# Performance work log

Hardware: AMD Instinct MI355X
Metric: run time of the kernel (lower is better)

## Reference

```python
import jax, jax.numpy as jnp
from jax import lax
import numpy as np

B, T, D, UNITS, NCLASSES = 256, 256, 512, 1024, 512


def setup_inputs() -> dict:
    key = jax.random.key(0)
    ks = jax.random.split(key, 6)
    x = jax.random.normal(ks[0], (B, T, D), dtype=jnp.float32)
    W = jax.random.normal(ks[1], (D + NCLASSES, 4 * UNITS), dtype=jnp.float32) * 0.02
    U = jax.random.normal(ks[2], (UNITS, 4 * UNITS), dtype=jnp.float32) * 0.02
    b = jnp.zeros((4 * UNITS,), dtype=jnp.float32)
    Wout = jax.random.normal(ks[3], (UNITS, NCLASSES), dtype=jnp.float32) * 0.02
    bout = jnp.zeros((NCLASSES,), dtype=jnp.float32)
    return {"x": x, "W": W, "U": U, "b": b, "Wout": Wout, "bout": bout}


def _hard_sigmoid(z):
    # Keras LSTM default recurrent activation
    return jnp.clip(0.2 * z + 0.5, 0.0, 1.0)


def reference(x, W, U, b, Wout, bout):
    units = U.shape[0]
    nclasses = Wout.shape[1]
    batch = x.shape[0]

    def step(carry, x_t):
        word_vec, h, c = carry
        ins = jnp.concatenate([x_t, word_vec], axis=1)          # [B, D+nclasses]
        z = ins @ W + h @ U + b                                  # [B, 4*units]
        zi, zf, zc, zo = jnp.split(z, 4, axis=1)
        c_new = _hard_sigmoid(zf) * c + _hard_sigmoid(zi) * jnp.tanh(zc)
        h_new = _hard_sigmoid(zo) * jnp.tanh(c_new)
        probs = jax.nn.softmax(h_new @ Wout + bout, axis=1)      # [B, nclasses]
        idx = jnp.argmax(probs, axis=1)                          # [B]
        new_word = jax.nn.one_hot(idx, nclasses, dtype=x_t.dtype)
        return (new_word, h_new, c_new), idx

    x_tmajor = jnp.swapaxes(x, 0, 1)                             # [T, B, D]
    # start_word = zeros_like(x_shuffled[0]) -> [B, D] (D == nclasses)
    init = (jnp.zeros((batch, x.shape[2]), x.dtype),
            jnp.zeros((batch, units), x.dtype),
            jnp.zeros((batch, units), x.dtype))
    _, idxs = lax.scan(step, init, x_tmajor)                     # [T, B]
    return jnp.swapaxes(idxs, 0, 1)                              # [B, T]
```

## Files before the change

### kernel.cpp

```cpp
#include <hip/hip_runtime.h>
#include <math.h>
#include <stdint.h>

#define Bn 256
#define Tn 256
#define Dn 512
#define UNITSn 1024
#define NCn 512
#define G4n 4096
#define KTn 1536
#define NT 48

typedef unsigned long long u64;
typedef __attribute__((ext_vector_type(4))) double d4;

__device__ __forceinline__ double hsigd(double z) {
    return fmin(fmax(0.2 * z + 0.5, 0.0), 1.0);
}

__device__ __forceinline__ u64 packlc(double v, int col) {
    double s = (v + 2048.0) * 1099511627776.0;
    u64 q = (u64)s;
    return (q << 10) | (u64)(1023 - col);
}

__global__ void convert_weights(const float* __restrict__ W, const float* __restrict__ U,
                                double* __restrict__ Wd)
{
    size_t stride = (size_t)gridDim.x * blockDim.x;
    for (size_t i = (size_t)blockIdx.x * blockDim.x + threadIdx.x;
         i < (size_t)KTn * G4n; i += stride) {
        int k = (int)(i >> 12);
        int j = (int)(i & 4095);
        float v = (k < Dn) ? W[i] : U[(size_t)(k - Dn) * G4n + j];
        Wd[i] = (double)v;
    }
}

#define AS_STR 34
#define BS_STR 34
#define AS_TILE (64 * AS_STR)
#define BS_TILE (32 * BS_STR)

__global__ __launch_bounds__(256, 2) void lstm_step_mfma(
    const float* __restrict__ x, const double* __restrict__ Wd,
    const float* __restrict__ W, const float* __restrict__ bias,
    const double* __restrict__ hin, double* __restrict__ hout,
    double* __restrict__ cst,
    const u64* __restrict__ slots_prev, u64* __restrict__ slots_cur,
    int* __restrict__ out, int t)
{
    __shared__ __align__(16) double smem[2 * AS_TILE + 2 * BS_TILE];

    const int tid = threadIdx.x;
    const int bid = blockIdx.x;
    const int ct_ = bid & 127;
    const int yt = bid >> 7;
    const int u0 = ct_ * 8;
    const int rowbase = yt * 64;

    if (ct_ == 0 && tid < 64) slots_cur[rowbase + tid] = 0ull;

    const int sr = tid >> 2;
    const int sk0 = (tid & 3) * 8;
    const int lb_k = tid >> 3;
    const int lb_c4 = (tid & 7) * 4;
    const int lb_gate = lb_c4 >> 3;
    const int lb_uoff = lb_c4 & 7;

    const float* xrow = x + (size_t)(rowbase + sr) * (Tn * Dn) + (size_t)t * Dn;
    const double* hrow = hin + (size_t)(rowbase + sr) * UNITSn;
    const double* wb = Wd + (size_t)lb_gate * UNITSn + u0 + lb_uoff;

    double apf[8];
    double2 bpf[2];

    auto prefetch = [&](int it) {
        int k0 = it * 32 + sk0;
        if (k0 < Dn) {
            float4 v0 = *(const float4*)(xrow + k0);
            float4 v1 = *(const float4*)(xrow + k0 + 4);
            apf[0] = (double)v0.x; apf[1] = (double)v0.y;
            apf[2] = (double)v0.z; apf[3] = (double)v0.w;
            apf[4] = (double)v1.x; apf[5] = (double)v1.y;
            apf[6] = (double)v1.z; apf[7] = (double)v1.w;
        } else {
            const double* hp = hrow + (k0 - Dn);
            double2 a = *(const double2*)(hp + 0);
            double2 b = *(const double2*)(hp + 2);
            double2 c2 = *(const double2*)(hp + 4);
            double2 d = *(const double2*)(hp + 6);
            apf[0] = a.x; apf[1] = a.y; apf[2] = b.x; apf[3] = b.y;
            apf[4] = c2.x; apf[5] = c2.y; apf[6] = d.x; apf[7] = d.y;
        }
        const double* bp = wb + (size_t)(it * 32 + lb_k) * G4n;
        bpf[0] = *(const double2*)(bp);
        bpf[1] = *(const double2*)(bp + 2);
    };
    auto store_tiles = [&](int p) {
        double* As = smem + p * AS_TILE;
        double* Bs = smem + 2 * AS_TILE + p * BS_TILE;
        #pragma unroll
        for (int j = 0; j < 8; j += 2) {
            double2 w2; w2.x = apf[j]; w2.y = apf[j + 1];
            *(double2*)&As[sr * AS_STR + sk0 + j] = w2;
        }
        *(double2*)&Bs[lb_k * BS_STR + lb_c4] = bpf[0];
        *(double2*)&Bs[lb_k * BS_STR + lb_c4 + 2] = bpf[1];
    };

    const int lane = tid & 63;
    const int wvi = tid >> 6;
    const int rs = wvi * 16;
    const int ml = lane & 15;
    const int kl = lane >> 4;

    d4 zero4 = {0.0, 0.0, 0.0, 0.0};
    double onek0 = (kl == 0) ? 1.0 : 0.0;
    double mk0   = (kl == 0) ? (double)ml : 0.0;
    d4 prow = __builtin_amdgcn_mfma_f64_16x16x4f64(mk0, onek0, zero4, 0, 0, 0);
    d4 pcol = __builtin_amdgcn_mfma_f64_16x16x4f64(onek0, mk0, zero4, 0, 0, 0);
    int zoff[4];
    #pragma unroll
    for (int r = 0; r < 4; r++)
        zoff[r] = (rs + (int)prow[r]) * 33 + (int)pcol[r];

    d4 acc[2];
    acc[0] = zero4; acc[1] = zero4;

    prefetch(0);
    store_tiles(0);
    __syncthreads();

    int p = 0;
    for (int it = 0; it < NT; it++) {
        if (it + 1 < NT) prefetch(it + 1);
        {
            const double* As = smem + p * AS_TILE;
            const double* Bs = smem + 2 * AS_TILE + p * BS_TILE;
            #pragma unroll
            for (int kq = 0; kq < 8; kq++) {
                double a = As[(rs + ml) * AS_STR + kq * 4 + kl];
                double b0 = Bs[(kq * 4 + kl) * BS_STR + ml];
                double b1 = Bs[(kq * 4 + kl) * BS_STR + 16 + ml];
                acc[0] = __builtin_amdgcn_mfma_f64_16x16x4f64(a, b0, acc[0], 0, 0, 0);
                acc[1] = __builtin_amdgcn_mfma_f64_16x16x4f64(a, b1, acc[1], 0, 0, 0);
            }
        }
        if (it + 1 < NT) store_tiles(p ^ 1);
        __syncthreads();
        p ^= 1;
    }

    double* zex = smem;
    #pragma unroll
    for (int r = 0; r < 4; r++) {
        zex[zoff[r]] = acc[0][r];
        zex[zoff[r] + 16] = acc[1][r];
    }
    __syncthreads();

    const int eu = tid & 7;
    const int rr = tid >> 3;
    const int ug = u0 + eu;
    const double bi0 = (double)bias[ug];
    const double bf0 = (double)bias[UNITSn + ug];
    const double bc0 = (double)bias[2 * UNITSn + ug];
    const double bo0 = (double)bias[3 * UNITSn + ug];

    #pragma unroll
    for (int s = 0; s < 2; s++) {
        int r = rr + 32 * s;
        int row = rowbase + r;
        double zi = zex[r * 33 + eu]      + bi0;
        double zf = zex[r * 33 + 8 + eu]  + bf0;
        double zc = zex[r * 33 + 16 + eu] + bc0;
        double zo = zex[r * 33 + 24 + eu] + bo0;
        if (t > 0) {
            u64 sp = slots_prev[row];
            int idx = 1023 - (int)(sp & 1023ull);
            const float* wrow = W + (size_t)(Dn + idx) * G4n + ug;
            zi += (double)wrow[0];
            zf += (double)wrow[UNITSn];
            zc += (double)wrow[2 * UNITSn];
            zo += (double)wrow[3 * UNITSn];
            if (ct_ == 0 && eu == 0) out[(size_t)row * Tn + (t - 1)] = idx;
        }
        size_t off = (size_t)row * UNITSn + ug;
        double cold = cst[off];
        double ig = hsigd(zi), fg = hsigd(zf), og = hsigd(zo);
        double cn = fg * cold + ig * tanh(zc);
        double hn = og * tanh(cn);
        cst[off] = cn;
        hout[off] = hn;
    }
}

__global__ __launch_bounds__(256, 2) void lstm_step(
    const float* __restrict__ x, const float* __restrict__ W,
    const float* __restrict__ U, const float* __restrict__ bias,
    const double* __restrict__ hin, double* __restrict__ hout,
    double* __restrict__ cst,
    const u64* __restrict__ slots_prev, u64* __restrict__ slots_cur,
    int* __restrict__ out, int t)
{
    __shared__ __align__(16) double smem[6144];

    const int tid = threadIdx.x;
    const int bid = blockIdx.x;
    const int ut = bid & 127;
    const int yt = bid >> 7;
    const int u0 = ut * 8;
    const int rowbase = yt * 64;

    if (ut == 0 && tid < 64) slots_cur[rowbase + tid] = 0ull;

    const int la_row = tid >> 2;
    const int la_k0 = (tid & 3) * 8;
    const int lb_k  = tid >> 3;
    const int lb_c4 = (tid & 7) * 4;
    const int lb_gate = lb_c4 >> 3;
    const int lb_uoff = lb_c4 & 7;

    const float* xrow = x + (size_t)(rowbase + la_row) * (Tn * Dn) + (size_t)t * Dn;
    const double* hrow = hin + (size_t)(rowbase + la_row) * UNITSn;

    double a_pf[8];
    double b_pf[4];

    auto prefetch = [&](int it) {
        int kg = it * 32;
        int k0 = kg + la_k0;
        if (k0 < Dn) {
            float4 v0 = *(const float4*)(xrow + k0);
            float4 v1 = *(const float4*)(xrow + k0 + 4);
            a_pf[0] = (double)v0.x; a_pf[1] = (double)v0.y;
            a_pf[2] = (double)v0.z; a_pf[3] = (double)v0.w;
            a_pf[4] = (double)v1.x; a_pf[5] = (double)v1.y;
            a_pf[6] = (double)v1.z; a_pf[7] = (double)v1.w;
        } else {
            const double* hp = hrow + (k0 - Dn);
            double2 h0v = *(const double2*)(hp + 0);
            double2 h1v = *(const double2*)(hp + 2);
            double2 h2v = *(const double2*)(hp + 4);
            double2 h3v = *(const double2*)(hp + 6);
            a_pf[0] = h0v.x; a_pf[1] = h0v.y; a_pf[2] = h1v.x; a_pf[3] = h1v.y;
            a_pf[4] = h2v.x; a_pf[5] = h2v.y; a_pf[6] = h3v.x; a_pf[7] = h3v.y;
        }
        int kB = kg + lb_k;
        const float* rowp = (kB < Dn) ? (W + (size_t)kB * G4n)
                                      : (U + (size_t)(kB - Dn) * G4n);
        float4 wv = *(const float4*)(rowp + lb_gate * UNITSn + u0 + lb_uoff);
        b_pf[0] = (double)wv.x; b_pf[1] = (double)wv.y;
        b_pf[2] = (double)wv.z; b_pf[3] = (double)wv.w;
    };
    auto store_tiles = [&](int p) {
        double* As = smem + p * 2048;
        double* Bs = smem + 4096 + p * 1024;
        #pragma unroll
        for (int j = 0; j < 8; j++) As[(la_k0 + j) * 64 + la_row] = a_pf[j];
        double2 w0; w0.x = b_pf[0]; w0.y = b_pf[1];
        double2 w1; w1.x = b_pf[2]; w1.y = b_pf[3];
        *(double2*)&Bs[lb_k * 32 + lb_c4] = w0;
        *(double2*)&Bs[lb_k * 32 + lb_c4 + 2] = w1;
    };

    const int lane = tid & 63;
    const int wv_ = tid >> 6;
    const int ri = lane >> 3;
    const int cj = lane & 7;
    const int rb = wv_ * 16 + ri * 2;

    double acc[2][4];
    #pragma unroll
    for (int i = 0; i < 2; i++)
        #pragma unroll
        for (int j = 0; j < 4; j++) acc[i][j] = 0.0;

    prefetch(0);
    store_tiles(0);
    __syncthreads();

    int p = 0;
    for (int it = 0; it < NT; it++) {
        if (it + 1 < NT) prefetch(it + 1);
        {
            const double* As = smem + p * 2048;
            const double* Bs = smem + 4096 + p * 1024;
            #pragma unroll
            for (int k = 0; k < 32; k++) {
                double2 a2 = *(const double2*)&As[k * 64 + rb];
                double2 b0 = *(const double2*)&Bs[k * 32 + cj * 4];
                double2 b1 = *(const double2*)&Bs[k * 32 + cj * 4 + 2];
                acc[0][0] = fma(a2.x, b0.x, acc[0][0]);
                acc[0][1] = fma(a2.x, b0.y, acc[0][1]);
                acc[0][2] = fma(a2.x, b1.x, acc[0][2]);
                acc[0][3] = fma(a2.x, b1.y, acc[0][3]);
                acc[1][0] = fma(a2.y, b0.x, acc[1][0]);
                acc[1][1] = fma(a2.y, b0.y, acc[1][1]);
                acc[1][2] = fma(a2.y, b1.x, acc[1][2]);
                acc[1][3] = fma(a2.y, b1.y, acc[1][3]);
            }
        }
        if (it + 1 < NT) store_tiles(p ^ 1);
        __syncthreads();
        p ^= 1;
    }

    double* zex = smem;
    #pragma unroll
    for (int i = 0; i < 2; i++) {
        double2 z0; z0.x = acc[i][0]; z0.y = acc[i][1];
        double2 z1; z1.x = acc[i][2]; z1.y = acc[i][3];
        *(double2*)&zex[(rb + i) * 32 + cj * 4] = z0;
        *(double2*)&zex[(rb + i) * 32 + cj * 4 + 2] = z1;
    }
    __syncthreads();

    const int eu = tid & 7;
    const int rr = tid >> 3;
    const int ug = u0 + eu;
    const double bi0 = (double)bias[ug];
    const double bf0 = (double)bias[UNITSn + ug];
    const double bc0 = (double)bias[2 * UNITSn + ug];
    const double bo0 = (double)bias[3 * UNITSn + ug];

    #pragma unroll
    for (int s = 0; s < 2; s++) {
        int r = rr + 32 * s;
        int row = rowbase + r;
        double zi = zex[r * 32 + eu]      + bi0;
        double zf = zex[r * 32 + 8 + eu]  + bf0;
        double zc = zex[r * 32 + 16 + eu] + bc0;
        double zo = zex[r * 32 + 24 + eu] + bo0;
        if (t > 0) {
            u64 sp = slots_prev[row];
            int idx = 1023 - (int)(sp & 1023ull);
            const float* wrow = W + (size_t)(Dn + idx) * G4n + ug;
            zi += (double)wrow[0];
            zf += (double)wrow[UNITSn];
            zc += (double)wrow[2 * UNITSn];
            zo += (double)wrow[3 * UNITSn];
            if (ut == 0 && eu == 0) out[(size_t)row * Tn + (t - 1)] = idx;
        }
        size_t off = (size_t)row * UNITSn + ug;
        double cold = cst[off];
        double ig = hsigd(zi), fg = hsigd(zf), og = hsigd(zo);
        double cn = fg * cold + ig * tanh(zc);
        double hn = og * tanh(cn);
        cst[off] = cn;
        hout[off] = hn;
    }
}

#define C_RT 8
#define C_CT 64
#define C_KC 32

__global__ __launch_bounds__(256) void logits_argmax(
    const double* __restrict__ h, const float* __restrict__ Wout,
    const float* __restrict__ bout, u64* __restrict__ slots)
{
    __shared__ double Hs[C_KC][9];
    __shared__ float  Ws[C_KC][C_CT];

    const int tid = threadIdx.x;
    const int ty = tid >> 5;
    const int tx = tid & 31;
    const int rbase = blockIdx.y * C_RT;
    const int cbase = blockIdx.x * C_CT;

    double acc0 = 0.0, acc1 = 0.0;

    const int lh_row = tid >> 5;
    const int lh_kk = tid & 31;
    const int lw_kk = tid >> 4;
    const int lw_j0 = (tid & 15) * 4;

    for (int kb = 0; kb < UNITSn; kb += C_KC) {
        Hs[lh_kk][lh_row] = h[(size_t)(rbase + lh_row) * UNITSn + kb + lh_kk];
        #pragma unroll
        for (int it = 0; it < 2; it++) {
            int kk = lw_kk + it * 16;
            float4 v = *(const float4*)(Wout + (size_t)(kb + kk) * NCn + cbase + lw_j0);
            *(float4*)&Ws[kk][lw_j0] = v;
        }
        __syncthreads();
        #pragma unroll
        for (int kk = 0; kk < C_KC; kk++) {
            double a = Hs[kk][ty];
            float2 wv = *(const float2*)&Ws[kk][tx * 2];
            acc0 = fma(a, (double)wv.x, acc0);
            acc1 = fma(a, (double)wv.y, acc1);
        }
        __syncthreads();
    }

    int col0 = cbase + tx * 2;
    double lg0 = acc0 + (double)bout[col0];
    double lg1 = acc1 + (double)bout[col0 + 1];

    u64 p0 = packlc(lg0, col0);
    u64 p1 = packlc(lg1, col0 + 1);
    u64 best = (p0 > p1) ? p0 : p1;
    #pragma unroll
    for (int off = 16; off >= 1; off >>= 1) {
        u64 o = __shfl_down(best, off, 32);
        if (o > best) best = o;
    }
    if (tx == 0) atomicMax(&slots[rbase + ty], best);
}

__global__ void final_decode(const u64* __restrict__ slots, int* __restrict__ out) {
    int b = threadIdx.x;
    u64 s = slots[b];
    out[(size_t)b * Tn + (Tn - 1)] = 1023 - (int)(s & 1023ull);
}

extern "C" void kernel_launch(void* const* d_in, const int* in_sizes, int n_in,
                              void* d_out, int out_size, void* d_ws, size_t ws_size,
                              hipStream_t stream) {
    const float* x    = (const float*)d_in[0];
    const float* W    = (const float*)d_in[1];
    const float* U    = (const float*)d_in[2];
    const float* bias = (const float*)d_in[3];
    const float* Wout = (const float*)d_in[4];
    const float* bout = (const float*)d_in[5];
    int* out = (int*)d_out;
    char* ws = (char*)d_ws;

    double* h0 = (double*)(ws);
    double* h1 = (double*)(ws + (2u << 20));
    double* c  = (double*)(ws + (4u << 20));
    u64* slots0 = (u64*)(ws + (6u << 20));
    u64* slots1 = (u64*)(ws + (6u << 20) + 2048);
    double* Wd  = (double*)(ws + (8u << 20));

    const size_t NEED = (8ull << 20) + (size_t)KTn * G4n * 8;
    const bool big = ws_size >= NEED;

    hipMemsetAsync(d_ws, 0, (6u << 20) + 4096, stream);
    if (big) convert_weights<<<1024, 256, 0, stream>>>(W, U, Wd);

    for (int t = 0; t < Tn; t++) {
        double* hin  = (t & 1) ? h1 : h0;
        double* hout = (t & 1) ? h0 : h1;
        u64* sprev = (t & 1) ? slots0 : slots1;
        u64* scur  = (t & 1) ? slots1 : slots0;
        if (big) {
            lstm_step_mfma<<<dim3(512), 256, 0, stream>>>(x, Wd, W, bias, hin, hout, c,
                                                          sprev, scur, out, t);
        } else {
            lstm_step<<<dim3(512), 256, 0, stream>>>(x, W, U, bias, hin, hout, c,
                                                     sprev, scur, out, t);
        }
        logits_argmax<<<dim3(8, 32), 256, 0, stream>>>(hout, Wout, bout, scur);
    }
    final_decode<<<1, Bn, 0, stream>>>(slots1, out);
}
```

Measured before the change: 31.28 ms.

## Swizzle LSTM block order, prefetch word-embedding rows, set MFMA priority, retile logits kernel

The LSTM step kernel now maps block IDs so that neighbouring blocks cover different column tiles, which changes L2 locality for the weight reads. It also loads the previous-step argmax slots at kernel start and issues the word-embedding row loads before the gate math, so their latency overlaps with other work. It raises wave priority around the MFMA inner loop with s_setprio. The logits/argmax kernel is retiled to 4 rows per block with one column per thread and a 64-wide xor-shuffle reduction, doubling the grid to expose more parallelism.

```diff
diff --git a/kernel.cpp b/kernel.cpp
--- a/kernel.cpp
+++ b/kernel.cpp
@@ -54,12 +54,21 @@
 
     const int tid = threadIdx.x;
     const int bid = blockIdx.x;
-    const int ct_ = bid & 127;
-    const int yt = bid >> 7;
+    const int ct_ = (bid & 7) * 16 + ((bid >> 3) & 15);
+    const int yt  = bid >> 7;
     const int u0 = ct_ * 8;
     const int rowbase = yt * 64;
 
     if (ct_ == 0 && tid < 64) slots_cur[rowbase + tid] = 0ull;
+
+    const int eu = tid & 7;
+    const int rr = tid >> 3;
+    const int ug = u0 + eu;
+    u64 spre0 = 0, spre1 = 0;
+    if (t > 0) {
+        spre0 = slots_prev[rowbase + rr];
+        spre1 = slots_prev[rowbase + rr + 32];
+    }
 
     const int sr = tid >> 2;
     const int sk0 = (tid & 3) * 8;
@@ -110,8 +119,7 @@
     };
 
     const int lane = tid & 63;
-    const int wvi = tid >> 6;
-    const int rs = wvi * 16;
+    const int rs = (tid >> 6) * 16;
     const int ml = lane & 15;
     const int kl = lane >> 4;
 
@@ -138,6 +146,7 @@
         {
             const double* As = smem + p * AS_TILE;
             const double* Bs = smem + 2 * AS_TILE + p * BS_TILE;
+            __builtin_amdgcn_s_setprio(1);
             #pragma unroll
             for (int kq = 0; kq < 8; kq++) {
                 double a = As[(rs + ml) * AS_STR + kq * 4 + kl];
@@ -146,6 +155,7 @@
                 acc[0] = __builtin_amdgcn_mfma_f64_16x16x4f64(a, b0, acc[0], 0, 0, 0);
                 acc[1] = __builtin_amdgcn_mfma_f64_16x16x4f64(a, b1, acc[1], 0, 0, 0);
             }
+            __builtin_amdgcn_s_setprio(0);
         }
         if (it + 1 < NT) store_tiles(p ^ 1);
         __syncthreads();
@@ -160,32 +170,33 @@
     }
     __syncthreads();
 
-    const int eu = tid & 7;
-    const int rr = tid >> 3;
-    const int ug = u0 + eu;
     const double bi0 = (double)bias[ug];
     const double bf0 = (double)bias[UNITSn + ug];
     const double bc0 = (double)bias[2 * UNITSn + ug];
     const double bo0 = (double)bias[3 * UNITSn + ug];
 
+    float wi0 = 0.f, wf0 = 0.f, wc0 = 0.f, wo0 = 0.f;
+    float wi1 = 0.f, wf1 = 0.f, wc1 = 0.f, wo1 = 0.f;
+    if (t > 0) {
+        int idx0 = 1023 - (int)(spre0 & 1023ull);
+        int idx1 = 1023 - (int)(spre1 & 1023ull);
+        const float* wr0 = W + (size_t)(Dn + idx0) * G4n + ug;
+        const float* wr1 = W + (size_t)(Dn + idx1) * G4n + ug;
+        wi0 = wr0[0]; wf0 = wr0[UNITSn]; wc0 = wr0[2 * UNITSn]; wo0 = wr0[3 * UNITSn];
+        wi1 = wr1[0]; wf1 = wr1[UNITSn]; wc1 = wr1[2 * UNITSn]; wo1 = wr1[3 * UNITSn];
+        if (ct_ == 0 && eu == 0) {
+            out[(size_t)(rowbase + rr) * Tn + (t - 1)] = idx0;
+            out[(size_t)(rowbase + rr + 32) * Tn + (t - 1)] = idx1;
+        }
+    }
     #pragma unroll
     for (int s = 0; s < 2; s++) {
         int r = rr + 32 * s;
         int row = rowbase + r;
-        double zi = zex[r * 33 + eu]      + bi0;
-        double zf = zex[r * 33 + 8 + eu]  + bf0;
-        double zc = zex[r * 33 + 16 + eu] + bc0;
-        double zo = zex[r * 33 + 24 + eu] + bo0;
-        if (t > 0) {
-            u64 sp = slots_prev[row];
-            int idx = 1023 - (int)(sp & 1023ull);
-            const float* wrow = W + (size_t)(Dn + idx) * G4n + ug;
-            zi += (double)wrow[0];
-            zf += (double)wrow[UNITSn];
-            zc += (double)wrow[2 * UNITSn];
-            zo += (double)wrow[3 * UNITSn];
-            if (ct_ == 0 && eu == 0) out[(size_t)row * Tn + (t - 1)] = idx;
-        }
+        double zi = zex[r * 33 + eu]      + bi0 + (double)(s ? wi1 : wi0);
+        double zf = zex[r * 33 + 8 + eu]  + bf0 + (double)(s ? wf1 : wf0);
+        double zc = zex[r * 33 + 16 + eu] + bc0 + (double)(s ? wc1 : wc0);
+        double zo = zex[r * 33 + 24 + eu] + bo0 + (double)(s ? wo1 : wo0);
         size_t off = (size_t)row * UNITSn + ug;
         double cold = cst[off];
         double ig = hsigd(zi), fg = hsigd(zf), og = hsigd(zo);
@@ -194,6 +205,57 @@
         cst[off] = cn;
         hout[off] = hn;
     }
+}
+
+__global__ __launch_bounds__(256) void logits_argmax(
+    const double* __restrict__ h, const float* __restrict__ Wout,
+    const float* __restrict__ bout, u64* __restrict__ slots)
+{
+    __shared__ double Hs[32][5];
+    __shared__ float  Ws[32][68];
+
+    const int tid = threadIdx.x;
+    const int row = tid >> 6;
+    const int col = tid & 63;
+    const int rbase = blockIdx.y * 4;
+    const int cbase = blockIdx.x * 64;
+
+    const int hr = tid >> 5;
+    const int hk = tid & 31;
+    const int wk = tid >> 3;
+    const int wj = (tid & 7) * 8;
+
+    double acc0 = 0.0, acc1 = 0.0;
+
+    for (int kb = 0; kb < UNITSn; kb += 32) {
+        if (tid < 128)
+            Hs[hk][hr] = h[(size_t)(rbase + hr) * UNITSn + kb + hk];
+        const float* wp = Wout + (size_t)(kb + wk) * NCn + cbase + wj;
+        *(float4*)&Ws[wk][wj]     = *(const float4*)(wp);
+        *(float4*)&Ws[wk][wj + 4] = *(const float4*)(wp + 4);
+        __syncthreads();
+        #pragma unroll
+        for (int kk = 0; kk < 32; kk += 2) {
+            acc0 = fma(Hs[kk][row],     (double)Ws[kk][col],     acc0);
+            acc1 = fma(Hs[kk + 1][row], (double)Ws[kk + 1][col], acc1);
+        }
+        __syncthreads();
+    }
+
+    double lg = acc0 + acc1 + (double)bout[cbase + col];
+    u64 best = packlc(lg, cbase + col);
+    #pragma unroll
+    for (int m = 32; m >= 1; m >>= 1) {
+        u64 o = __shfl_xor(best, m, 64);
+        if (o > best) best = o;
+    }
+    if (col == 0) atomicMax(&slots[rbase + row], best);
+}
+
+__global__ void final_decode(const u64* __restrict__ slots, int* __restrict__ out) {
+    int b = threadIdx.x;
+    u64 s = slots[b];
+    out[(size_t)b * Tn + (Tn - 1)] = 1023 - (int)(s & 1023ull);
 }
 
 __global__ __launch_bounds__(256, 2) void lstm_step(
@@ -353,70 +415,6 @@
     }
 }
 
-#define C_RT 8
-#define C_CT 64
-#define C_KC 32
-
-__global__ __launch_bounds__(256) void logits_argmax(
-    const double* __restrict__ h, const float* __restrict__ Wout,
-    const float* __restrict__ bout, u64* __restrict__ slots)
-{
-    __shared__ double Hs[C_KC][9];
-    __shared__ float  Ws[C_KC][C_CT];
-
-    const int tid = threadIdx.x;
-    const int ty = tid >> 5;
-    const int tx = tid & 31;
-    const int rbase = blockIdx.y * C_RT;
-    const int cbase = blockIdx.x * C_CT;
-
-    double acc0 = 0.0, acc1 = 0.0;
-
-    const int lh_row = tid >> 5;
-    const int lh_kk = tid & 31;
-    const int lw_kk = tid >> 4;
-    const int lw_j0 = (tid & 15) * 4;
-
-    for (int kb = 0; kb < UNITSn; kb += C_KC) {
-        Hs[lh_kk][lh_row] = h[(size_t)(rbase + lh_row) * UNITSn + kb + lh_kk];
-        #pragma unroll
-        for (int it = 0; it < 2; it++) {
-            int kk = lw_kk + it * 16;
-            float4 v = *(const float4*)(Wout + (size_t)(kb + kk) * NCn + cbase + lw_j0);
-            *(float4*)&Ws[kk][lw_j0] = v;
-        }
-        __syncthreads();
-        #pragma unroll
-        for (int kk = 0; kk < C_KC; kk++) {
-            double a = Hs[kk][ty];
-            float2 wv = *(const float2*)&Ws[kk][tx * 2];
-            acc0 = fma(a, (double)wv.x, acc0);
-            acc1 = fma(a, (double)wv.y, acc1);
-        }
-        __syncthreads();
-    }
-
-    int col0 = cbase + tx * 2;
-    double lg0 = acc0 + (double)bout[col0];
-    double lg1 = acc1 + (double)bout[col0 + 1];
-
-    u64 p0 = packlc(lg0, col0);
-    u64 p1 = packlc(lg1, col0 + 1);
-    u64 best = (p0 > p1) ? p0 : p1;
-    #pragma unroll
-    for (int off = 16; off >= 1; off >>= 1) {
-        u64 o = __shfl_down(best, off, 32);
-        if (o > best) best = o;
-    }
-    if (tx == 0) atomicMax(&slots[rbase + ty], best);
-}
-
-__global__ void final_decode(const u64* __restrict__ slots, int* __restrict__ out) {
-    int b = threadIdx.x;
-    u64 s = slots[b];
-    out[(size_t)b * Tn + (Tn - 1)] = 1023 - (int)(s & 1023ull);
-}
-
 extern "C" void kernel_launch(void* const* d_in, const int* in_sizes, int n_in,
                               void* d_out, int out_size, void* d_ws, size_t ws_size,
                               hipStream_t stream) {
@@ -454,7 +452,7 @@
             lstm_step<<<dim3(512), 256, 0, stream>>>(x, W, U, bias, hin, hout, c,
                                                      sprev, scur, out, t);
         }
-        logits_argmax<<<dim3(8, 32), 256, 0, stream>>>(hout, Wout, bout, scur);
+        logits_argmax<<<dim3(8, 64), 256, 0, stream>>>(hout, Wout, bout, scur);
     }
     final_decode<<<1, Bn, 0, stream>>>(slots1, out);
 }
```

Measured after the change: 33.27 ms. +6.4%, slower.
